# Kernel optimization log

Hardware: AMD Instinct MI355X
Metric: run time of the kernel (lower is better)

The kernel has to match this reference:

```python
import jax, jax.numpy as jnp
import numpy as np
from math import sqrt

B, L, D, H, DK, IN = 128, 256, 128, 4, 64, 40
N = B * L
E = 524288
NLAYERS = 4
DISW = 1.5
EPS = 1e-5


def _ln(x, g, b):
    mu = x.mean(-1, keepdims=True)
    v = ((x - mu) ** 2).mean(-1, keepdims=True)
    return (x - mu) / jnp.sqrt(v + EPS) * g + b


def setup_inputs() -> dict:
    key = jax.random.key(0)
    ks = jax.random.split(key, 32)
    x = jax.random.normal(ks[0], (N, IN), jnp.float32)
    # equal-sized graphs: graph g owns nodes [g*L, (g+1)*L)
    e_per = E // B
    off = (jnp.arange(E) // e_per) * L
    src = off + jax.random.randint(ks[1], (E,), 0, L)
    dst = off + jax.random.randint(ks[2], (E,), 0, L)
    edge_index = jnp.stack([src, dst]).astype(jnp.int32)
    edge_attr = jax.random.uniform(ks[3], (E,), jnp.float32)
    # adjacency-type matrix with entries in {0, 1, 1.2} as in the source's adj semantics
    a = jax.random.randint(ks[4], (B, L, L), 0, 3)
    adj = jnp.where(a == 2, 1.2, a.astype(jnp.float32))
    dis = jax.random.randint(ks[5], (B, L, L), 0, 7).astype(jnp.float32)
    mask = jnp.ones((B, L), dtype=bool)  # all graphs have length L -> no padding
    s = 0.05
    p = {}
    p['gnn0_rel_w'] = jax.random.normal(ks[6], (IN, D)) * s
    p['gnn0_rel_b'] = jnp.zeros((D,), jnp.float32)
    p['gnn0_root_w'] = jax.random.normal(ks[7], (IN, D)) * s
    p['gnn_rel_w'] = jax.random.normal(ks[8], (NLAYERS - 1, D, D)) * s
    p['gnn_rel_b'] = jnp.zeros((NLAYERS - 1, D), jnp.float32)
    p['gnn_root_w'] = jax.random.normal(ks[9], (NLAYERS - 1, D, D)) * s
    p['nm_g'] = jnp.ones((NLAYERS, D), jnp.float32)
    p['nm_b'] = jnp.zeros((NLAYERS, D), jnp.float32)
    p['wq'] = jax.random.normal(ks[10], (NLAYERS, D, H * DK)) * s
    p['wk'] = jax.random.normal(ks[11], (NLAYERS, D, H * DK)) * s
    p['wv'] = jax.random.normal(ks[12], (NLAYERS, D, H * DK)) * s
    p['fc'] = jax.random.normal(ks[13], (NLAYERS, H * DK, D)) * s
    p['mha_ln_g'] = jnp.ones((NLAYERS, D), jnp.float32)
    p['mha_ln_b'] = jnp.zeros((NLAYERS, D), jnp.float32)
    p['enc_ln_g'] = jnp.ones((NLAYERS, D), jnp.float32)
    p['enc_ln_b'] = jnp.zeros((NLAYERS, D), jnp.float32)
    p['proj_w'] = jax.random.normal(ks[14], (D, D)) * s
    p['proj_b'] = jnp.zeros((D,), jnp.float32)
    return dict(x=x, edge_index=edge_index, edge_attr=edge_attr, adj=adj, dis=dis, mask=mask, **p)


def _graph_conv(x, src, dst, ew, rel_w, rel_b, root_w):
    # torch_geometric GraphConv: lin_rel(sum_j e_ji * x_j) + lin_root(x_i)
    msg = ew[:, None] * x[src]
    agg = jax.ops.segment_sum(msg, dst, num_segments=N)
    return agg @ rel_w + rel_b + x @ root_w


def _encoder(xb, pad, matrix, wq, wk, wv, fc, mg, mb, eg, eb):
    q = (xb @ wq).reshape(B, L, H, DK).transpose(0, 2, 1, 3)  # [B,H,L,dk]
    k = (xb @ wk).reshape(B, L, H, DK).transpose(0, 2, 1, 3)
    v = (xb @ wv).reshape(B, L, H, DK).transpose(0, 2, 1, 3)
    scores = jnp.einsum('bhqd,bhkd->bhqk', q, k) / sqrt(DK) * matrix[:, None]
    scores = jnp.where(pad[:, None, None, :], -1e9, scores)
    attn = jax.nn.softmax(scores, axis=-1)
    ctx = jnp.einsum('bhqk,bhkd->bhqd', attn, v).transpose(0, 2, 1, 3).reshape(B, L, H * DK)
    out = _ln(ctx @ fc, mg, mb)  # MHA output LayerNorm (dropout is eval -> identity)
    return _ln(out + xb, eg, eb)  # EncoderLayer residual + LayerNorm


def reference(x, edge_index, edge_attr, adj, dis, mask,
              gnn0_rel_w, gnn0_rel_b, gnn0_root_w,
              gnn_rel_w, gnn_rel_b, gnn_root_w,
              nm_g, nm_b, wq, wk, wv, fc,
              mha_ln_g, mha_ln_b, enc_ln_g, enc_ln_b,
              proj_w, proj_b):
    src, dst = edge_index[0], edge_index[1]
    # matrix construction (done once; same matrix_pad reused every layer)
    adj_ = jnp.where(adj == 1.2, 1.1, adj)
    dis_ = jnp.where(dis == 0.0, 0.0, 1.0 / jnp.power(DISW, dis - 1.0))
    matrix = jnp.where(adj == 0.0, dis_, adj_)  # [B,L,L]
    pad = ~mask  # key padding mask (True = masked); all-False here
    h = x
    for i in range(NLAYERS):
        rw = gnn0_rel_w if i == 0 else gnn_rel_w[i - 1]
        rb = gnn0_rel_b if i == 0 else gnn_rel_b[i - 1]
        ow = gnn0_root_w if i == 0 else gnn_root_w[i - 1]
        h = _graph_conv(h, src, dst, edge_attr, rw, rb, ow)
        h = jax.nn.relu(_ln(h, nm_g[i], nm_b[i]))
        xb = h.reshape(B, L, D)  # to_dense_batch with equal lengths
        xb = _encoder(xb, pad, matrix, wq[i], wk[i], wv[i], fc[i],
                      mha_ln_g[i], mha_ln_b[i], enc_ln_g[i], enc_ln_b[i])
        h = xb.reshape(N, D)  # masked_select back to node list
    return h @ proj_w + proj_b
```

## Files before the change

### kernel.cpp

```cpp
#include <hip/hip_runtime.h>
#include <stdint.h>

typedef unsigned short u16;
typedef unsigned int u32;
typedef __attribute__((ext_vector_type(4))) float f32x4;
typedef __attribute__((ext_vector_type(8))) short bf16x8;

#define NB 128
#define LL 256
#define DD 128
#define EDGES 524288
#define EPG 4096
#define NN (NB*LL)

__device__ __forceinline__ float bf2f(u16 u) {
    union { u32 i; float f; } v; v.i = ((u32)u) << 16; return v.f;
}
__device__ __forceinline__ u16 f2bf(float f) {
    union { float f; u32 i; } v; v.f = f;
    u32 i = v.i;
    u32 r = (i + 0x7fffu + ((i >> 16) & 1u)) >> 16;
    return (u16)r;
}
__device__ __forceinline__ float matfn(float a, float dv) {
    if (a != 0.f) return (a == 1.2f) ? 1.1f : a;
    return (dv == 0.f) ? 0.f : exp2f((1.f - dv) * 0.5849625007211562f);
}
__device__ __forceinline__ float red16(float v) {
#pragma unroll
    for (int off = 1; off < 16; off <<= 1) v += __shfl_xor(v, off, 64);
    return v;
}
__device__ __forceinline__ u32 cvtpk(float lo, float hi) {
    u32 r;
    asm("v_cvt_pk_bf16_f32 %0, %1, %2" : "=v"(r) : "v"(lo), "v"(hi));
    return r;
}
__device__ __forceinline__ u32 bperm(int srcLane, u32 v) {
    return (u32)__builtin_amdgcn_ds_bpermute(srcLane << 2, (int)v);
}


__global__ __launch_bounds__(256) void scatter_w_k(const int* __restrict__ srcI,
                                                   const int* __restrict__ dstI,
                                                   const float* __restrict__ ew,
                                                   float* __restrict__ Wf) {
    int e = blockIdx.x * 256 + threadIdx.x;
    if (e >= EDGES) return;
    int b = e >> 12;
    atomicAdd(&Wf[(size_t)b * 65536 + (size_t)(dstI[e] & 255) * 256 + (srcI[e] & 255)], ew[e]);
}

__global__ __launch_bounds__(256) void cast_w_k(const float* __restrict__ Wf, u16* __restrict__ Wb) {
    int i = blockIdx.x * 256 + threadIdx.x;
    float4 v = ((const float4*)Wf)[i];
    ushort4 o;
    o.x = f2bf(v.x); o.y = f2bf(v.y); o.z = f2bf(v.z); o.w = f2bf(v.w);
    ((ushort4*)Wb)[i] = o;
}

__global__ __launch_bounds__(256) void build_matrix_k(const float* __restrict__ adj,
                                                      const float* __restrict__ dis,
                                                      float* __restrict__ mat) {
    int i = blockIdx.x * 256 + threadIdx.x;
    mat[i] = 0.125f * matfn(adj[i], dis[i]);
}

__global__ __launch_bounds__(256) void prep_weights_k(
        const float* __restrict__ g0_rel_w, const float* __restrict__ g0_root_w,
        const float* __restrict__ g_rel_w,  const float* __restrict__ g_root_w,
        const float* __restrict__ wq, const float* __restrict__ wk,
        const float* __restrict__ wv, const float* __restrict__ fc,
        const float* __restrict__ proj_w,
        u16* __restrict__ wconvT0, u16* __restrict__ wconvT,
        u16* __restrict__ wqkvT, u16* __restrict__ fcT, u16* __restrict__ projT) {
    int i = blockIdx.x * 256 + threadIdx.x;
    if (i < 16384) {
        int m = i >> 7, k = i & 127;
        float v = 0.f;
        if (k < 40) v = g0_rel_w[k * 128 + m];
        else if (k >= 64 && k < 104) v = g0_root_w[(k - 64) * 128 + m];
        wconvT0[i] = f2bf(v);
        return;
    }
    i -= 16384;
    if (i < 98304) {
        int l = i >> 15, jj = i & 32767;
        int m = jj >> 8, k = jj & 255;
        float v = (k < 128) ? g_rel_w[l * 16384 + k * 128 + m]
                            : g_root_w[l * 16384 + (k - 128) * 128 + m];
        wconvT[i] = f2bf(v);
        return;
    }
    i -= 98304;
    if (i < 393216) {
        int l = i / 98304, jj = i % 98304;
        int m = jj >> 7, k = jj & 127;
        const float* s = (m < 256) ? wq : (m < 512) ? wk : wv;
        int mm = m & 255;
        wqkvT[i] = f2bf(s[l * 32768 + k * 256 + mm]);
        return;
    }
    i -= 393216;
    if (i < 131072) {
        int l = i >> 15, jj = i & 32767;
        int m = jj >> 8, k = jj & 255;
        fcT[i] = f2bf(fc[l * 32768 + k * 128 + m]);
        return;
    }
    i -= 131072;
    {
        int m = i >> 7, k = i & 127;
        projT[i] = f2bf(proj_w[k * 128 + m]);
    }
}

__global__ __launch_bounds__(256) void transpose_x_k(const float* __restrict__ x,
                                                     u16* __restrict__ hT) {
    int gw = blockIdx.x * 4 + (threadIdx.x >> 6);
    int lane = threadIdx.x & 63;
    int b = gw >> 6, rem = gw & 63, db = rem >> 5, jb = rem & 31;
    int d = (db << 6) + lane;
    u16 vals[8];
#pragma unroll
    for (int jj = 0; jj < 8; ++jj) {
        int node = (b << 8) + (jb << 3) + jj;
        vals[jj] = (d < 40) ? f2bf(x[(size_t)node * 40 + d]) : (u16)0;
    }
    *(uint4*)(hT + (size_t)b * 32768 + (size_t)d * 256 + (jb << 3)) = *(uint4*)vals;
}


template<bool IS0>
__global__ __launch_bounds__(256) void gemm_agg(const u16* __restrict__ Wb,
                                                const u16* __restrict__ BT0,
                                                const float* __restrict__ x,
                                                u16* __restrict__ Aagg) {
    __shared__ __align__(16) u16 lds[8192];
    char* ldsc = (char*)lds;
    int t = threadIdx.x, lane = t & 63, wid = t >> 6;
    int b = blockIdx.x >> 1, rt = blockIdx.x & 1;
    int row0 = rt << 7, nbase = b << 8;
    const u16* A = Wb + (size_t)b * 65536 + (size_t)row0 * 256;
    const u16* BT = BT0 + (size_t)b * 32768;

    f32x4 zero = {0.f, 0.f, 0.f, 0.f};
    f32x4 acc[4][4];
#pragma unroll
    for (int mt = 0; mt < 4; ++mt)
#pragma unroll
        for (int nt = 0; nt < 4; ++nt) acc[mt][nt] = zero;

    int wr = wid >> 1, wc = wid & 1;
    int rA = wr * 64 + (lane & 15);
    int rB = wc * 64 + (lane & 15);
    int kch = (lane >> 4) << 4;

    for (int kt = 0; kt < 8; ++kt) {
        int kc = kt << 5;
#pragma unroll
        for (int i = 0; i < 2; ++i) {
            int off = wid * 2048 + i * 1024 + lane * 16;
            int r = off >> 6, cb = off & 63;
            __builtin_amdgcn_global_load_lds((const u32*)((const char*)A + ((size_t)r * 256 + kc) * 2 + cb),
                                             (u32*)(ldsc + wid * 2048 + i * 1024), 16, 0, 0);
            __builtin_amdgcn_global_load_lds((const u32*)((const char*)BT + ((size_t)r * 256 + kc) * 2 + cb),
                                             (u32*)(ldsc + 8192 + wid * 2048 + i * 1024), 16, 0, 0);
        }
        __syncthreads();
        bf16x8 af[4], bfr[4];
#pragma unroll
        for (int mt = 0; mt < 4; ++mt)
            af[mt] = *(const bf16x8*)(ldsc + (rA + mt * 16) * 64 + kch);
#pragma unroll
        for (int nt = 0; nt < 4; ++nt)
            bfr[nt] = *(const bf16x8*)(ldsc + 8192 + (rB + nt * 16) * 64 + kch);
#pragma unroll
        for (int mt = 0; mt < 4; ++mt)
#pragma unroll
            for (int nt = 0; nt < 4; ++nt)
                acc[mt][nt] = __builtin_amdgcn_mfma_f32_16x16x32_bf16(af[mt], bfr[nt], acc[mt][nt], 0, 0, 0);
        __syncthreads();
    }

    int colb = wc * 64 + (lane & 15);
    int rowb = wr * 64 + ((lane >> 4) << 2);
#pragma unroll
    for (int mt = 0; mt < 4; ++mt)
#pragma unroll
        for (int nt = 0; nt < 4; ++nt)
#pragma unroll
            for (int r = 0; r < 4; ++r)
                Aagg[(size_t)(nbase + row0 + rowb + mt * 16 + r) * 128 + colb + nt * 16]
                    = f2bf(acc[mt][nt][r]);
    if (IS0) {
        for (int idx = t; idx < 128 * 40; idx += 256) {
            int i = idx / 40, c = idx - i * 40;
            int node = nbase + row0 + i;
            Aagg[(size_t)node * 128 + 64 + c] = f2bf(x[(size_t)node * 40 + c]);
        }
    }
}


__global__ __launch_bounds__(256) void gemm_qkv(const u16* __restrict__ A,
                                                const u16* __restrict__ BT,
                                                u16* __restrict__ qP,
                                                u16* __restrict__ kP,
                                                u16* __restrict__ vT) {
    __shared__ __align__(16) u16 lds[8192];
    char* ldsc = (char*)lds;
    int t = threadIdx.x, lane = t & 63, wid = t >> 6;
    int row0 = blockIdx.x * 128, col0 = blockIdx.y * 128;

    f32x4 zero = {0.f, 0.f, 0.f, 0.f};
    f32x4 acc[4][4];
#pragma unroll
    for (int mt = 0; mt < 4; ++mt)
#pragma unroll
        for (int nt = 0; nt < 4; ++nt) acc[mt][nt] = zero;

    int wr = wid >> 1, wc = wid & 1;
    int rA = wr * 64 + (lane & 15);
    int rB = wc * 64 + (lane & 15);
    int kch = (lane >> 4) << 4;

    for (int kt = 0; kt < 4; ++kt) {
        int kc = kt << 5;
#pragma unroll
        for (int i = 0; i < 2; ++i) {
            int off = wid * 2048 + i * 1024 + lane * 16;
            int r = off >> 6, cb = off & 63;
            __builtin_amdgcn_global_load_lds((const u32*)((const char*)A + ((size_t)(row0 + r) * 128 + kc) * 2 + cb),
                                             (u32*)(ldsc + wid * 2048 + i * 1024), 16, 0, 0);
            __builtin_amdgcn_global_load_lds((const u32*)((const char*)BT + ((size_t)(col0 + r) * 128 + kc) * 2 + cb),
                                             (u32*)(ldsc + 8192 + wid * 2048 + i * 1024), 16, 0, 0);
        }
        __syncthreads();
        bf16x8 af[4], bfr[4];
#pragma unroll
        for (int mt = 0; mt < 4; ++mt)
            af[mt] = *(const bf16x8*)(ldsc + (rA + mt * 16) * 64 + kch);
#pragma unroll
        for (int nt = 0; nt < 4; ++nt)
            bfr[nt] = *(const bf16x8*)(ldsc + 8192 + (rB + nt * 16) * 64 + kch);
#pragma unroll
        for (int mt = 0; mt < 4; ++mt)
#pragma unroll
            for (int nt = 0; nt < 4; ++nt)
                acc[mt][nt] = __builtin_amdgcn_mfma_f32_16x16x32_bf16(af[mt], bfr[nt], acc[mt][nt], 0, 0, 0);
        __syncthreads();
    }

    int colb = col0 + wc * 64 + (lane & 15);
    int rowb = row0 + wr * 64 + ((lane >> 4) << 2);
    int bb = row0 >> 8;
    if (col0 < 512) {
        u16* dst = (col0 < 256) ? qP : kP;
#pragma unroll
        for (int mt = 0; mt < 4; ++mt) {
#pragma unroll
            for (int nt = 0; nt < 4; ++nt) {
                int c = (colb + nt * 16) & 255;
                int hh = c >> 6, d = c & 63;
#pragma unroll
                for (int r = 0; r < 4; ++r) {
                    int node = (rowb + mt * 16 + r) & 255;
                    dst[(size_t)(bb * 4 + hh) * 16384 + node * 64 + d] = f2bf(acc[mt][nt][r]);
                }
            }
        }
    } else {
#pragma unroll
        for (int mt = 0; mt < 4; ++mt) {
            int node0 = (rowb + mt * 16) & 255;
#pragma unroll
            for (int nt = 0; nt < 4; ++nt) {
                int c = colb + nt * 16 - 512;
                int hh = c >> 6, d = c & 63;
                u16 tmp[4];
#pragma unroll
                for (int r = 0; r < 4; ++r) tmp[r] = f2bf(acc[mt][nt][r]);
                *(ushort4*)(vT + (size_t)(bb * 4 + hh) * 16384 + d * 256 + node0) = *(ushort4*)tmp;
            }
        }
    }
}


__global__ __launch_bounds__(256) void gemm_proj(const u16* __restrict__ A,
                                                 const u16* __restrict__ BT,
                                                 float* __restrict__ Out,
                                                 const float* __restrict__ bias) {
    __shared__ __align__(16) u16 lds[8192];
    char* ldsc = (char*)lds;
    int t = threadIdx.x, lane = t & 63, wid = t >> 6;
    int row0 = blockIdx.x * 128;

    f32x4 zero = {0.f, 0.f, 0.f, 0.f};
    f32x4 acc[4][4];
#pragma unroll
    for (int mt = 0; mt < 4; ++mt)
#pragma unroll
        for (int nt = 0; nt < 4; ++nt) acc[mt][nt] = zero;

    int wr = wid >> 1, wc = wid & 1;
    int rA = wr * 64 + (lane & 15);
    int rB = wc * 64 + (lane & 15);
    int kch = (lane >> 4) << 4;

    for (int kt = 0; kt < 4; ++kt) {
        int kc = kt << 5;
#pragma unroll
        for (int i = 0; i < 2; ++i) {
            int off = wid * 2048 + i * 1024 + lane * 16;
            int r = off >> 6, cb = off & 63;
            __builtin_amdgcn_global_load_lds((const u32*)((const char*)A + ((size_t)(row0 + r) * 128 + kc) * 2 + cb),
                                             (u32*)(ldsc + wid * 2048 + i * 1024), 16, 0, 0);
            __builtin_amdgcn_global_load_lds((const u32*)((const char*)BT + ((size_t)r * 128 + kc) * 2 + cb),
                                             (u32*)(ldsc + 8192 + wid * 2048 + i * 1024), 16, 0, 0);
        }
        __syncthreads();
        bf16x8 af[4], bfr[4];
#pragma unroll
        for (int mt = 0; mt < 4; ++mt)
            af[mt] = *(const bf16x8*)(ldsc + (rA + mt * 16) * 64 + kch);
#pragma unroll
        for (int nt = 0; nt < 4; ++nt)
            bfr[nt] = *(const bf16x8*)(ldsc + 8192 + (rB + nt * 16) * 64 + kch);
#pragma unroll
        for (int mt = 0; mt < 4; ++mt)
#pragma unroll
            for (int nt = 0; nt < 4; ++nt)
                acc[mt][nt] = __builtin_amdgcn_mfma_f32_16x16x32_bf16(af[mt], bfr[nt], acc[mt][nt], 0, 0, 0);
        __syncthreads();
    }

    int colb = wc * 64 + (lane & 15);
    int rowb = row0 + wr * 64 + ((lane >> 4) << 2);
#pragma unroll
    for (int mt = 0; mt < 4; ++mt)
#pragma unroll
        for (int nt = 0; nt < 4; ++nt)
#pragma unroll
            for (int r = 0; r < 4; ++r)
                Out[(size_t)(rowb + mt * 16 + r) * 128 + colb + nt * 16] =
                    acc[mt][nt][r] + bias[colb + nt * 16];
}


__global__ __launch_bounds__(256) void gemm_conv_ln0(const u16* __restrict__ A,
                                                     const u16* __restrict__ BT,
                                                     const float* __restrict__ rb,
                                                     const float* __restrict__ g,
                                                     const float* __restrict__ be,
                                                     u16* __restrict__ hout) {
    __shared__ __align__(16) u16 lds[8192];
    char* ldsc = (char*)lds;
    int t = threadIdx.x, lane = t & 63, wid = t >> 6;
    int row0 = blockIdx.x * 128;

    f32x4 zero = {0.f, 0.f, 0.f, 0.f};
    f32x4 acc[4][4];
#pragma unroll
    for (int mt = 0; mt < 4; ++mt)
#pragma unroll
        for (int nt = 0; nt < 4; ++nt) acc[mt][nt] = zero;

    int wr = wid >> 1, wc = wid & 1;
    int rA = wr * 64 + (lane & 15);
    int rB = wc * 64 + (lane & 15);
    int kch = (lane >> 4) << 4;

    for (int kt = 0; kt < 4; ++kt) {
        int kc = kt << 5;
#pragma unroll
        for (int i = 0; i < 2; ++i) {
            int off = wid * 2048 + i * 1024 + lane * 16;
            int r = off >> 6, cb = off & 63;
            __builtin_amdgcn_global_load_lds((const u32*)((const char*)A + ((size_t)(row0 + r) * 128 + kc) * 2 + cb),
                                             (u32*)(ldsc + wid * 2048 + i * 1024), 16, 0, 0);
            __builtin_amdgcn_global_load_lds((const u32*)((const char*)BT + ((size_t)r * 128 + kc) * 2 + cb),
                                             (u32*)(ldsc + 8192 + wid * 2048 + i * 1024), 16, 0, 0);
        }
        __syncthreads();
        bf16x8 af[4], bfr[4];
#pragma unroll
        for (int mt = 0; mt < 4; ++mt)
            af[mt] = *(const bf16x8*)(ldsc + (rA + mt * 16) * 64 + kch);
#pragma unroll
        for (int nt = 0; nt < 4; ++nt)
            bfr[nt] = *(const bf16x8*)(ldsc + 8192 + (rB + nt * 16) * 64 + kch);
#pragma unroll
        for (int mt = 0; mt < 4; ++mt)
#pragma unroll
            for (int nt = 0; nt < 4; ++nt)
                acc[mt][nt] = __builtin_amdgcn_mfma_f32_16x16x32_bf16(af[mt], bfr[nt], acc[mt][nt], 0, 0, 0);
        __syncthreads();
    }

    float* redS = (float*)ldsc;
    float* redQ = (float*)(ldsc + 2048);
    int colbase = wc * 64 + (lane & 15);
    int qrow = (lane >> 4) << 2;
    float rbv[4], gv[4], bev[4];
#pragma unroll
    for (int nt = 0; nt < 4; ++nt) {
        int c = colbase + nt * 16;
        rbv[nt] = rb[c]; gv[nt] = g[c]; bev[nt] = be[c];
    }
#pragma unroll
    for (int mt = 0; mt < 4; ++mt)
#pragma unroll
        for (int r = 0; r < 4; ++r) {
            float s = 0.f, q = 0.f;
#pragma unroll
            for (int nt = 0; nt < 4; ++nt) {
                float v = acc[mt][nt][r] + rbv[nt];
                s += v; q += v * v;
            }
            s = red16(s); q = red16(q);
            if ((lane & 15) == 0) {
                int lr = wr * 64 + qrow + mt * 16 + r;
                redS[lr * 2 + wc] = s; redQ[lr * 2 + wc] = q;
            }
        }
    __syncthreads();
#pragma unroll
    for (int mt = 0; mt < 4; ++mt)
#pragma unroll
        for (int r = 0; r < 4; ++r) {
            int lr = wr * 64 + qrow + mt * 16 + r;
            float mu = (redS[lr * 2] + redS[lr * 2 + 1]) * (1.f / 128.f);
            float var = (redQ[lr * 2] + redQ[lr * 2 + 1]) * (1.f / 128.f) - mu * mu;
            float rs = rsqrtf(var + 1e-5f);
            size_t rbase = (size_t)(row0 + lr) * 128;
#pragma unroll
            for (int nt = 0; nt < 4; ++nt) {
                float v = acc[mt][nt][r] + rbv[nt];
                float o = (v - mu) * rs * gv[nt] + bev[nt];
                o = o < 0.f ? 0.f : o;
                hout[rbase + colbase + nt * 16] = f2bf(o);
            }
        }
}


__global__ __launch_bounds__(256) void gemm_conv_ln_split(const u16* __restrict__ Aagg,
                                                          u16* h,
                                                          const u16* __restrict__ BT,
                                                          const float* __restrict__ rb,
                                                          const float* __restrict__ g,
                                                          const float* __restrict__ be) {
    __shared__ __align__(16) u16 lds[8192];
    char* ldsc = (char*)lds;
    int t = threadIdx.x, lane = t & 63, wid = t >> 6;
    int row0 = blockIdx.x * 128;

    f32x4 zero = {0.f, 0.f, 0.f, 0.f};
    f32x4 acc[4][4];
#pragma unroll
    for (int mt = 0; mt < 4; ++mt)
#pragma unroll
        for (int nt = 0; nt < 4; ++nt) acc[mt][nt] = zero;

    int wr = wid >> 1, wc = wid & 1;
    int rA = wr * 64 + (lane & 15);
    int rB = wc * 64 + (lane & 15);
    int kch = (lane >> 4) << 4;

    for (int kt = 0; kt < 8; ++kt) {
        const u16* Abase = (kt < 4) ? Aagg : (const u16*)h;
        int kcl = (kt & 3) << 5;
        int kc = kt << 5;
#pragma unroll
        for (int i = 0; i < 2; ++i) {
            int off = wid * 2048 + i * 1024 + lane * 16;
            int r = off >> 6, cb = off & 63;
            __builtin_amdgcn_global_load_lds((const u32*)((const char*)Abase + ((size_t)(row0 + r) * 128 + kcl) * 2 + cb),
                                             (u32*)(ldsc + wid * 2048 + i * 1024), 16, 0, 0);
            __builtin_amdgcn_global_load_lds((const u32*)((const char*)BT + ((size_t)r * 256 + kc) * 2 + cb),
                                             (u32*)(ldsc + 8192 + wid * 2048 + i * 1024), 16, 0, 0);
        }
        __syncthreads();
        bf16x8 af[4], bfr[4];
#pragma unroll
        for (int mt = 0; mt < 4; ++mt)
            af[mt] = *(const bf16x8*)(ldsc + (rA + mt * 16) * 64 + kch);
#pragma unroll
        for (int nt = 0; nt < 4; ++nt)
            bfr[nt] = *(const bf16x8*)(ldsc + 8192 + (rB + nt * 16) * 64 + kch);
#pragma unroll
        for (int mt = 0; mt < 4; ++mt)
#pragma unroll
            for (int nt = 0; nt < 4; ++nt)
                acc[mt][nt] = __builtin_amdgcn_mfma_f32_16x16x32_bf16(af[mt], bfr[nt], acc[mt][nt], 0, 0, 0);
        __syncthreads();
    }

    float* redS = (float*)ldsc;
    float* redQ = (float*)(ldsc + 2048);
    int colbase = wc * 64 + (lane & 15);
    int qrow = (lane >> 4) << 2;
    float rbv[4], gv[4], bev[4];
#pragma unroll
    for (int nt = 0; nt < 4; ++nt) {
        int c = colbase + nt * 16;
        rbv[nt] = rb[c]; gv[nt] = g[c]; bev[nt] = be[c];
    }
#pragma unroll
    for (int mt = 0; mt < 4; ++mt)
#pragma unroll
        for (int r = 0; r < 4; ++r) {
            float s = 0.f, q = 0.f;
#pragma unroll
            for (int nt = 0; nt < 4; ++nt) {
                float v = acc[mt][nt][r] + rbv[nt];
                s += v; q += v * v;
            }
            s = red16(s); q = red16(q);
            if ((lane & 15) == 0) {
                int lr = wr * 64 + qrow + mt * 16 + r;
                redS[lr * 2 + wc] = s; redQ[lr * 2 + wc] = q;
            }
        }
    __syncthreads();
#pragma unroll
    for (int mt = 0; mt < 4; ++mt)
#pragma unroll
        for (int r = 0; r < 4; ++r) {
            int lr = wr * 64 + qrow + mt * 16 + r;
            float mu = (redS[lr * 2] + redS[lr * 2 + 1]) * (1.f / 128.f);
            float var = (redQ[lr * 2] + redQ[lr * 2 + 1]) * (1.f / 128.f) - mu * mu;
            float rs = rsqrtf(var + 1e-5f);
            size_t rbase = (size_t)(row0 + lr) * 128;
#pragma unroll
            for (int nt = 0; nt < 4; ++nt) {
                float v = acc[mt][nt][r] + rbv[nt];
                float o = (v - mu) * rs * gv[nt] + bev[nt];
                o = o < 0.f ? 0.f : o;
                h[rbase + colbase + nt * 16] = f2bf(o);
            }
        }
}


__global__ __launch_bounds__(256) void gemm_fc_ln2(const u16* __restrict__ A,
                                                   const u16* __restrict__ BT,
                                                   const float* __restrict__ mg,
                                                   const float* __restrict__ mb,
                                                   const float* __restrict__ eg,
                                                   const float* __restrict__ eb,
                                                   u16* __restrict__ h,
                                                   u16* __restrict__ hT) {
    __shared__ __align__(16) u16 lds[8192];
    char* ldsc = (char*)lds;
    int t = threadIdx.x, lane = t & 63, wid = t >> 6;
    int row0 = blockIdx.x * 128;

    f32x4 zero = {0.f, 0.f, 0.f, 0.f};
    f32x4 acc[4][4];
#pragma unroll
    for (int mt = 0; mt < 4; ++mt)
#pragma unroll
        for (int nt = 0; nt < 4; ++nt) acc[mt][nt] = zero;

    int wr = wid >> 1, wc = wid & 1;
    int rA = wr * 64 + (lane & 15);
    int rB = wc * 64 + (lane & 15);
    int kch = (lane >> 4) << 4;

    for (int kt = 0; kt < 8; ++kt) {
        int kc = kt << 5;
#pragma unroll
        for (int i = 0; i < 2; ++i) {
            int off = wid * 2048 + i * 1024 + lane * 16;
            int r = off >> 6, cb = off & 63;
            __builtin_amdgcn_global_load_lds((const u32*)((const char*)A + ((size_t)(row0 + r) * 256 + kc) * 2 + cb),
                                             (u32*)(ldsc + wid * 2048 + i * 1024), 16, 0, 0);
            __builtin_amdgcn_global_load_lds((const u32*)((const char*)BT + ((size_t)r * 256 + kc) * 2 + cb),
                                             (u32*)(ldsc + 8192 + wid * 2048 + i * 1024), 16, 0, 0);
        }
        __syncthreads();
        bf16x8 af[4], bfr[4];
#pragma unroll
        for (int mt = 0; mt < 4; ++mt)
            af[mt] = *(const bf16x8*)(ldsc + (rA + mt * 16) * 64 + kch);
#pragma unroll
        for (int nt = 0; nt < 4; ++nt)
            bfr[nt] = *(const bf16x8*)(ldsc + 8192 + (rB + nt * 16) * 64 + kch);
#pragma unroll
        for (int mt = 0; mt < 4; ++mt)
#pragma unroll
            for (int nt = 0; nt < 4; ++nt)
                acc[mt][nt] = __builtin_amdgcn_mfma_f32_16x16x32_bf16(af[mt], bfr[nt], acc[mt][nt], 0, 0, 0);
        __syncthreads();
    }

    float* redS  = (float*)ldsc;
    float* redQ  = (float*)(ldsc + 2048);
    float* redS2 = (float*)(ldsc + 4096);
    float* redQ2 = (float*)(ldsc + 6144);
    int colbase = wc * 64 + (lane & 15);
    int qrow = (lane >> 4) << 2;
    float mgv[4], mbv[4], egv[4], ebv[4];
#pragma unroll
    for (int nt = 0; nt < 4; ++nt) {
        int c = colbase + nt * 16;
        mgv[nt] = mg[c]; mbv[nt] = mb[c]; egv[nt] = eg[c]; ebv[nt] = eb[c];
    }
#pragma unroll
    for (int mt = 0; mt < 4; ++mt)
#pragma unroll
        for (int r = 0; r < 4; ++r) {
            float s = 0.f, q = 0.f;
#pragma unroll
            for (int nt = 0; nt < 4; ++nt) {
                float v = acc[mt][nt][r];
                s += v; q += v * v;
            }
            s = red16(s); q = red16(q);
            if ((lane & 15) == 0) {
                int lr = wr * 64 + qrow + mt * 16 + r;
                redS[lr * 2 + wc] = s; redQ[lr * 2 + wc] = q;
            }
        }
    __syncthreads();
#pragma unroll
    for (int mt = 0; mt < 4; ++mt)
#pragma unroll
        for (int r = 0; r < 4; ++r) {
            int lr = wr * 64 + qrow + mt * 16 + r;
            float mu = (redS[lr * 2] + redS[lr * 2 + 1]) * (1.f / 128.f);
            float var = (redQ[lr * 2] + redQ[lr * 2 + 1]) * (1.f / 128.f) - mu * mu;
            float rs = rsqrtf(var + 1e-5f);
            size_t rbase = (size_t)(row0 + lr) * 128;
            float s2 = 0.f, q2 = 0.f;
#pragma unroll
            for (int nt = 0; nt < 4; ++nt) {
                float o = (acc[mt][nt][r] - mu) * rs * mgv[nt] + mbv[nt];
                float z = o + bf2f(h[rbase + colbase + nt * 16]);
                acc[mt][nt][r] = z;
                s2 += z; q2 += z * z;
            }
            s2 = red16(s2); q2 = red16(q2);
            if ((lane & 15) == 0) {
                redS2[lr * 2 + wc] = s2; redQ2[lr * 2 + wc] = q2;
            }
        }
    __syncthreads();
    int bb = row0 >> 8;
#pragma unroll
    for (int mt = 0; mt < 4; ++mt) {
        u16 tvals[4][4];
#pragma unroll
        for (int r = 0; r < 4; ++r) {
            int lr = wr * 64 + qrow + mt * 16 + r;
            float mu = (redS2[lr * 2] + redS2[lr * 2 + 1]) * (1.f / 128.f);
            float var = (redQ2[lr * 2] + redQ2[lr * 2 + 1]) * (1.f / 128.f) - mu * mu;
            float rs = rsqrtf(var + 1e-5f);
            size_t rbase = (size_t)(row0 + lr) * 128;
#pragma unroll
            for (int nt = 0; nt < 4; ++nt) {
                float z = acc[mt][nt][r];
                u16 o = f2bf((z - mu) * rs * egv[nt] + ebv[nt]);
                h[rbase + colbase + nt * 16] = o;
                tvals[nt][r] = o;
            }
        }
        int node0 = ((row0 & 255) + wr * 64 + qrow + mt * 16);
#pragma unroll
        for (int nt = 0; nt < 4; ++nt) {
            int d = colbase + nt * 16;
            *(ushort4*)(hT + (size_t)bb * 32768 + (size_t)d * 256 + node0) = *(ushort4*)tvals[nt];
        }
    }
}


__global__ __launch_bounds__(512) void attn_k(const u16* __restrict__ qP,
                                              const u16* __restrict__ kP,
                                              const u16* __restrict__ vT,
                                              const float* __restrict__ mat,
                                              u16* __restrict__ ctx) {
    __shared__ __align__(16) u16 Kl[256 * 72];
    __shared__ __align__(16) u16 Vl[64 * 264];
    int t = threadIdx.x, lane = t & 63, w = t >> 6;
    int b = blockIdx.x, hh = blockIdx.y;
    int bh = b * 4 + hh;
    int lg = lane >> 4, q16 = lane & 15;

    {
        const u16* kb = kP + (size_t)bh * 16384;
#pragma unroll
        for (int i = 0; i < 4; ++i) {
            int idx = i * 512 + t;
            int node = idx >> 3, oct = idx & 7;
            *(uint4*)(Kl + node * 72 + oct * 8) = *(const uint4*)(kb + node * 64 + oct * 8);
        }
        const u16* vb = vT + (size_t)bh * 16384;
#pragma unroll
        for (int i = 0; i < 4; ++i) {
            int idx = i * 512 + t;
            int d = idx >> 5, p = idx & 31;
            *(uint4*)(Vl + d * 264 + p * 8) = *(const uint4*)(vb + d * 256 + p * 8);
        }
    }
    __syncthreads();

    f32x4 zero = {0.f, 0.f, 0.f, 0.f};
    bool loA = (lg < 2);
    int s01 = q16 + ((lg & 1) << 5);
    int s23 = s01 + 16;

    for (int qi = 0; qi < 2; ++qi) {
        int qrow_l = w * 32 + qi * 16;

        const u16* qsrc = qP + (size_t)bh * 16384 + (qrow_l + q16) * 64 + (lg << 3);
        bf16x8 aq0 = *(const bf16x8*)(qsrc);
        bf16x8 aq1 = *(const bf16x8*)(qsrc + 32);

        f32x4 sc[16];
#pragma unroll
        for (int nt = 0; nt < 16; ++nt) {
            const u16* ks = Kl + (nt * 16 + q16) * 72 + (lg << 3);
            bf16x8 k0 = *(const bf16x8*)(ks);
            bf16x8 k1 = *(const bf16x8*)(ks + 32);
            f32x4 a = __builtin_amdgcn_mfma_f32_16x16x32_bf16(k0, aq0, zero, 0, 0, 0);
            a = __builtin_amdgcn_mfma_f32_16x16x32_bf16(k1, aq1, a, 0, 0, 0);
            sc[nt] = a;
        }

        const float* mrow = mat + ((size_t)b * LL + qrow_l + q16) * LL + (lg << 2);
#pragma unroll
        for (int nt = 0; nt < 16; ++nt) {
            f32x4 mv = *(const f32x4*)(mrow + nt * 16);
#pragma unroll
            for (int r = 0; r < 4; ++r)
                sc[nt][r] *= mv[r];
        }

        float mx = -1e30f;
#pragma unroll
        for (int nt = 0; nt < 16; ++nt)
#pragma unroll
            for (int r = 0; r < 4; ++r) mx = fmaxf(mx, sc[nt][r]);
        mx = fmaxf(mx, __shfl_xor(mx, 16, 64));
        mx = fmaxf(mx, __shfl_xor(mx, 32, 64));
        float sm = 0.f;
#pragma unroll
        for (int nt = 0; nt < 16; ++nt)
#pragma unroll
            for (int r = 0; r < 4; ++r) {
                float e = __expf(sc[nt][r] - mx);
                sc[nt][r] = e;
                sm += e;
            }
        sm += __shfl_xor(sm, 16, 64);
        sm += __shfl_xor(sm, 32, 64);
        float inv = 1.f / sm;
#pragma unroll
        for (int nt = 0; nt < 16; ++nt)
#pragma unroll
            for (int r = 0; r < 4; ++r) sc[nt][r] *= inv;

        f32x4 oa[4];
#pragma unroll
        for (int dt = 0; dt < 4; ++dt) oa[dt] = zero;
#pragma unroll
        for (int kt = 0; kt < 8; ++kt) {
            u32 A0 = cvtpk(sc[2 * kt][0], sc[2 * kt][1]);
            u32 A1 = cvtpk(sc[2 * kt][2], sc[2 * kt][3]);
            u32 B0 = cvtpk(sc[2 * kt + 1][0], sc[2 * kt + 1][1]);
            u32 B1 = cvtpk(sc[2 * kt + 1][2], sc[2 * kt + 1][3]);
            u32 a0s = bperm(s01, A0), b0s = bperm(s01, B0);
            u32 a1s = bperm(s01, A1), b1s = bperm(s01, B1);
            u32 a0t = bperm(s23, A0), b0t = bperm(s23, B0);
            u32 a1t = bperm(s23, A1), b1t = bperm(s23, B1);
            union { u32 u[4]; bf16x8 v; } pa;
            pa.u[0] = loA ? a0s : b0s;
            pa.u[1] = loA ? a1s : b1s;
            pa.u[2] = loA ? a0t : b0t;
            pa.u[3] = loA ? a1t : b1t;
#pragma unroll
            for (int dt = 0; dt < 4; ++dt) {
                bf16x8 bv = *(const bf16x8*)(Vl + (dt * 16 + q16) * 264 + kt * 32 + (lg << 3));
                oa[dt] = __builtin_amdgcn_mfma_f32_16x16x32_bf16(pa.v, bv, oa[dt], 0, 0, 0);
            }
        }
#pragma unroll
        for (int dt = 0; dt < 4; ++dt)
#pragma unroll
            for (int r = 0; r < 4; ++r)
                ctx[(size_t)(b * LL + qrow_l + (lg << 2) + r) * 256 + hh * 64 + dt * 16 + q16] = f2bf(oa[dt][r]);
    }
}


extern "C" void kernel_launch(void* const* d_in, const int* in_sizes, int n_in,
                              void* d_out, int out_size, void* d_ws, size_t ws_size,
                              hipStream_t stream) {
    (void)out_size; (void)ws_size; (void)n_in;
    const float* x        = (const float*)d_in[0];
    const int*   ei       = (const int*)d_in[1];
    const float* ea       = (const float*)d_in[2];
    const float* adj      = (const float*)d_in[3];
    const float* dis      = (const float*)d_in[4];
    int pb = (in_sizes[5] == 5120) ? 5 : 6;
    const float* g0_rel_w = (const float*)d_in[pb + 0];
    const float* g0_rel_b = (const float*)d_in[pb + 1];
    const float* g0_root_w= (const float*)d_in[pb + 2];
    const float* g_rel_w  = (const float*)d_in[pb + 3];
    const float* g_rel_b  = (const float*)d_in[pb + 4];
    const float* g_root_w = (const float*)d_in[pb + 5];
    const float* nm_g     = (const float*)d_in[pb + 6];
    const float* nm_b     = (const float*)d_in[pb + 7];
    const float* wq       = (const float*)d_in[pb + 8];
    const float* wk       = (const float*)d_in[pb + 9];
    const float* wv       = (const float*)d_in[pb + 10];
    const float* fc       = (const float*)d_in[pb + 11];
    const float* mha_g    = (const float*)d_in[pb + 12];
    const float* mha_b    = (const float*)d_in[pb + 13];
    const float* enc_g    = (const float*)d_in[pb + 14];
    const float* enc_b    = (const float*)d_in[pb + 15];
    const float* proj_w   = (const float*)d_in[pb + 16];
    const float* proj_b   = (const float*)d_in[pb + 17];
    const int* srcI = ei;
    const int* dstI = ei + EDGES;

    char* w = (char*)d_ws;
    float* Wf     = (float*)w; w += (size_t)33554432;
    u16*   Acat   = (u16*)w;   w += (size_t)16777216;
    u16*   h      = (u16*)w;   w += (size_t)8388608;
    u16*   qP     = (u16*)w;   w += (size_t)16777216;
    u16*   kP     = (u16*)w;   w += (size_t)16777216;
    u16*   Wb     = (u16*)w;   w += (size_t)16777216;
    u16*   bigT   = (u16*)w;   w += (size_t)16777216;
    u16* wconvT0  = (u16*)w;   w += (size_t)32768;
    u16* wconvT   = (u16*)w;   w += (size_t)196608;
    u16* wqkvT    = (u16*)w;   w += (size_t)786432;
    u16* fcT      = (u16*)w;   w += (size_t)262144;
    u16* projT    = (u16*)w;   w += (size_t)32768;
    float* mat = Wf;
    u16*   ctx = Acat;
    u16*   hT  = bigT;
    u16*   vT  = bigT;

    hipMemsetAsync(Wf, 0, 33554432, stream);
    scatter_w_k<<<2048, 256, 0, stream>>>(srcI, dstI, ea, Wf);
    cast_w_k<<<8192, 256, 0, stream>>>(Wf, Wb);
    build_matrix_k<<<32768, 256, 0, stream>>>(adj, dis, mat);
    prep_weights_k<<<2560, 256, 0, stream>>>(g0_rel_w, g0_root_w, g_rel_w, g_root_w,
                                             wq, wk, wv, fc, proj_w,
                                             wconvT0, wconvT, wqkvT, fcT, projT);
    transpose_x_k<<<2048, 256, 0, stream>>>(x, hT);

    for (int L = 0; L < 4; ++L) {
        if (L == 0) {
            gemm_agg<true><<<256, 256, 0, stream>>>(Wb, hT, x, Acat);
            gemm_conv_ln0<<<256, 256, 0, stream>>>(Acat, wconvT0, g0_rel_b, nm_g, nm_b, h);
        } else {
            gemm_agg<false><<<256, 256, 0, stream>>>(Wb, hT, x, Acat);
            gemm_conv_ln_split<<<256, 256, 0, stream>>>(Acat, h, wconvT + (L - 1) * 32768,
                                                        g_rel_b + (L - 1) * 128,
                                                        nm_g + L * 128, nm_b + L * 128);
        }
        gemm_qkv<<<dim3(256, 6), 256, 0, stream>>>(h, wqkvT + L * 98304, qP, kP, vT);
        attn_k<<<dim3(NB, 4), 512, 0, stream>>>(qP, kP, vT, mat, ctx);
        gemm_fc_ln2<<<256, 256, 0, stream>>>(ctx, fcT + L * 32768,
                                             mha_g + L * 128, mha_b + L * 128,
                                             enc_g + L * 128, enc_b + L * 128, h, hT);
    }
    gemm_proj<<<256, 256, 0, stream>>>(h, projT, (float*)d_out, proj_b);
}
```

Measured before the change: 521.6 us.

## Fuse aggregation GEMM with conv GEMM+LayerNorm and store attention matrix in bf16

The aggregation GEMM output now stays in LDS and feeds directly into the conv GEMM, bias, LayerNorm and ReLU inside one kernel. This removes the intermediate Acat round trip through global memory and one launch per layer. Separately, the attention bias matrix is stored as bf16 instead of fp32, halving its read traffic in attn_k at some cost in precision. The larger LDS footprint may reduce occupancy.

```diff
diff --git a/kernel.cpp b/kernel.cpp
--- a/kernel.cpp
+++ b/kernel.cpp
@@ -61,9 +61,9 @@
 
 __global__ __launch_bounds__(256) void build_matrix_k(const float* __restrict__ adj,
                                                       const float* __restrict__ dis,
-                                                      float* __restrict__ mat) {
+                                                      u16* __restrict__ matB) {
     int i = blockIdx.x * 256 + threadIdx.x;
-    mat[i] = 0.125f * matfn(adj[i], dis[i]);
+    matB[i] = f2bf(0.125f * matfn(adj[i], dis[i]));
 }
 
 __global__ __launch_bounds__(256) void prep_weights_k(
@@ -132,12 +132,17 @@
 
 
 template<bool IS0>
-__global__ __launch_bounds__(256) void gemm_agg(const u16* __restrict__ Wb,
-                                                const u16* __restrict__ BT0,
-                                                const float* __restrict__ x,
-                                                u16* __restrict__ Aagg) {
-    __shared__ __align__(16) u16 lds[8192];
+__global__ __launch_bounds__(256) void gemm_agg_conv(const u16* __restrict__ Wb,
+                                                     const u16* __restrict__ BT0,
+                                                     const float* __restrict__ x,
+                                                     u16* h,
+                                                     const u16* __restrict__ BTc,
+                                                     const float* __restrict__ rb,
+                                                     const float* __restrict__ g,
+                                                     const float* __restrict__ be) {
+    __shared__ __align__(16) u16 lds[8192 + 128 * 136];
     char* ldsc = (char*)lds;
+    u16* aggT = lds + 8192;
     int t = threadIdx.x, lane = t & 63, wid = t >> 6;
     int b = blockIdx.x >> 1, rt = blockIdx.x & 1;
     int row0 = rt << 7, nbase = b << 8;
@@ -183,23 +188,113 @@
         __syncthreads();
     }
 
-    int colb = wc * 64 + (lane & 15);
-    int rowb = wr * 64 + ((lane >> 4) << 2);
-#pragma unroll
-    for (int mt = 0; mt < 4; ++mt)
+    {
+        int colb = wc * 64 + (lane & 15);
+        int rowb = wr * 64 + ((lane >> 4) << 2);
+#pragma unroll
+        for (int mt = 0; mt < 4; ++mt)
+#pragma unroll
+            for (int nt = 0; nt < 4; ++nt)
+#pragma unroll
+                for (int r = 0; r < 4; ++r)
+                    aggT[(rowb + mt * 16 + r) * 136 + colb + nt * 16] = f2bf(acc[mt][nt][r]);
+        if (IS0) {
+            for (int idx = t; idx < 128 * 40; idx += 256) {
+                int i = idx / 40, c = idx - i * 40;
+                aggT[i * 136 + 64 + c] = f2bf(x[(size_t)(nbase + row0 + i) * 40 + c]);
+            }
+        }
+    }
+    __syncthreads();
+
+#pragma unroll
+    for (int mt = 0; mt < 4; ++mt)
+#pragma unroll
+        for (int nt = 0; nt < 4; ++nt) acc[mt][nt] = zero;
+
+    const int NKT = IS0 ? 4 : 8;
+    const int KK = IS0 ? 128 : 256;
+    for (int kt = 0; kt < NKT; ++kt) {
+        int kc = kt << 5;
+        bool fromLds = IS0 || (kt < 4);
+#pragma unroll
+        for (int i = 0; i < 2; ++i) {
+            int off = wid * 2048 + i * 1024 + lane * 16;
+            int r = off >> 6, cb = off & 63;
+            if (!fromLds) {
+                int kcl = (kt - 4) << 5;
+                __builtin_amdgcn_global_load_lds((const u32*)((const char*)h + ((size_t)(nbase + row0 + r) * 128 + kcl) * 2 + cb),
+                                                 (u32*)(ldsc + wid * 2048 + i * 1024), 16, 0, 0);
+            }
+            __builtin_amdgcn_global_load_lds((const u32*)((const char*)BTc + ((size_t)r * KK + kc) * 2 + cb),
+                                             (u32*)(ldsc + 8192 + wid * 2048 + i * 1024), 16, 0, 0);
+        }
+        __syncthreads();
+        bf16x8 af[4], bfr[4];
+        if (fromLds) {
+#pragma unroll
+            for (int mt = 0; mt < 4; ++mt)
+                af[mt] = *(const bf16x8*)((const char*)aggT + (rA + mt * 16) * 272 + kt * 64 + kch);
+        } else {
+#pragma unroll
+            for (int mt = 0; mt < 4; ++mt)
+                af[mt] = *(const bf16x8*)(ldsc + (rA + mt * 16) * 64 + kch);
+        }
 #pragma unroll
         for (int nt = 0; nt < 4; ++nt)
-#pragma unroll
-            for (int r = 0; r < 4; ++r)
-                Aagg[(size_t)(nbase + row0 + rowb + mt * 16 + r) * 128 + colb + nt * 16]
-                    = f2bf(acc[mt][nt][r]);
-    if (IS0) {
-        for (int idx = t; idx < 128 * 40; idx += 256) {
-            int i = idx / 40, c = idx - i * 40;
-            int node = nbase + row0 + i;
-            Aagg[(size_t)node * 128 + 64 + c] = f2bf(x[(size_t)node * 40 + c]);
-        }
-    }
+            bfr[nt] = *(const bf16x8*)(ldsc + 8192 + (rB + nt * 16) * 64 + kch);
+#pragma unroll
+        for (int mt = 0; mt < 4; ++mt)
+#pragma unroll
+            for (int nt = 0; nt < 4; ++nt)
+                acc[mt][nt] = __builtin_amdgcn_mfma_f32_16x16x32_bf16(af[mt], bfr[nt], acc[mt][nt], 0, 0, 0);
+        __syncthreads();
+    }
+
+    float* redS = (float*)ldsc;
+    float* redQ = (float*)(ldsc + 2048);
+    int colbase = wc * 64 + (lane & 15);
+    int qrow = (lane >> 4) << 2;
+    float rbv[4], gv[4], bev[4];
+#pragma unroll
+    for (int nt = 0; nt < 4; ++nt) {
+        int c = colbase + nt * 16;
+        rbv[nt] = rb[c]; gv[nt] = g[c]; bev[nt] = be[c];
+    }
+#pragma unroll
+    for (int mt = 0; mt < 4; ++mt)
+#pragma unroll
+        for (int r = 0; r < 4; ++r) {
+            float s = 0.f, q = 0.f;
+#pragma unroll
+            for (int nt = 0; nt < 4; ++nt) {
+                float v = acc[mt][nt][r] + rbv[nt];
+                s += v; q += v * v;
+            }
+            s = red16(s); q = red16(q);
+            if ((lane & 15) == 0) {
+                int lr = wr * 64 + qrow + mt * 16 + r;
+                redS[lr * 2 + wc] = s; redQ[lr * 2 + wc] = q;
+            }
+        }
+    __syncthreads();
+#pragma unroll
+    for (int mt = 0; mt < 4; ++mt)
+#pragma unroll
+        for (int r = 0; r < 4; ++r) {
+            int lr = wr * 64 + qrow + mt * 16 + r;
+            float mu = (redS[lr * 2] + redS[lr * 2 + 1]) * (1.f / 128.f);
+            float var = (redQ[lr * 2] + redQ[lr * 2 + 1]) * (1.f / 128.f) - mu * mu;
+            float rs = rsqrtf(var + 1e-5f);
+            size_t rbase = (size_t)(nbase + row0 + lr) * 128;
+#pragma unroll
+            for (int nt = 0; nt < 4; ++nt) {
+                float v = acc[mt][nt][r] + rbv[nt];
+                float o = (v - mu) * rs * gv[nt] + bev[nt];
+                o = o < 0.f ? 0.f : o;
+                h[rbase + colbase + nt * 16] = f2bf(o);
+            }
+        }
 }
 
 
@@ -346,202 +441,6 @@
             for (int r = 0; r < 4; ++r)
                 Out[(size_t)(rowb + mt * 16 + r) * 128 + colb + nt * 16] =
                     acc[mt][nt][r] + bias[colb + nt * 16];
-}
-
-
-__global__ __launch_bounds__(256) void gemm_conv_ln0(const u16* __restrict__ A,
-                                                     const u16* __restrict__ BT,
-                                                     const float* __restrict__ rb,
-                                                     const float* __restrict__ g,
-                                                     const float* __restrict__ be,
-                                                     u16* __restrict__ hout) {
-    __shared__ __align__(16) u16 lds[8192];
-    char* ldsc = (char*)lds;
-    int t = threadIdx.x, lane = t & 63, wid = t >> 6;
-    int row0 = blockIdx.x * 128;
-
-    f32x4 zero = {0.f, 0.f, 0.f, 0.f};
-    f32x4 acc[4][4];
-#pragma unroll
-    for (int mt = 0; mt < 4; ++mt)
-#pragma unroll
-        for (int nt = 0; nt < 4; ++nt) acc[mt][nt] = zero;
-
-    int wr = wid >> 1, wc = wid & 1;
-    int rA = wr * 64 + (lane & 15);
-    int rB = wc * 64 + (lane & 15);
-    int kch = (lane >> 4) << 4;
-
-    for (int kt = 0; kt < 4; ++kt) {
-        int kc = kt << 5;
-#pragma unroll
-        for (int i = 0; i < 2; ++i) {
-            int off = wid * 2048 + i * 1024 + lane * 16;
-            int r = off >> 6, cb = off & 63;
-            __builtin_amdgcn_global_load_lds((const u32*)((const char*)A + ((size_t)(row0 + r) * 128 + kc) * 2 + cb),
-                                             (u32*)(ldsc + wid * 2048 + i * 1024), 16, 0, 0);
-            __builtin_amdgcn_global_load_lds((const u32*)((const char*)BT + ((size_t)r * 128 + kc) * 2 + cb),
-                                             (u32*)(ldsc + 8192 + wid * 2048 + i * 1024), 16, 0, 0);
-        }
-        __syncthreads();
-        bf16x8 af[4], bfr[4];
-#pragma unroll
-        for (int mt = 0; mt < 4; ++mt)
-            af[mt] = *(const bf16x8*)(ldsc + (rA + mt * 16) * 64 + kch);
-#pragma unroll
-        for (int nt = 0; nt < 4; ++nt)
-            bfr[nt] = *(const bf16x8*)(ldsc + 8192 + (rB + nt * 16) * 64 + kch);
-#pragma unroll
-        for (int mt = 0; mt < 4; ++mt)
-#pragma unroll
-            for (int nt = 0; nt < 4; ++nt)
-                acc[mt][nt] = __builtin_amdgcn_mfma_f32_16x16x32_bf16(af[mt], bfr[nt], acc[mt][nt], 0, 0, 0);
-        __syncthreads();
-    }
-
-    float* redS = (float*)ldsc;
-    float* redQ = (float*)(ldsc + 2048);
-    int colbase = wc * 64 + (lane & 15);
-    int qrow = (lane >> 4) << 2;
-    float rbv[4], gv[4], bev[4];
-#pragma unroll
-    for (int nt = 0; nt < 4; ++nt) {
-        int c = colbase + nt * 16;
-        rbv[nt] = rb[c]; gv[nt] = g[c]; bev[nt] = be[c];
-    }
-#pragma unroll
-    for (int mt = 0; mt < 4; ++mt)
-#pragma unroll
-        for (int r = 0; r < 4; ++r) {
-            float s = 0.f, q = 0.f;
-#pragma unroll
-            for (int nt = 0; nt < 4; ++nt) {
-                float v = acc[mt][nt][r] + rbv[nt];
-                s += v; q += v * v;
-            }
-            s = red16(s); q = red16(q);
-            if ((lane & 15) == 0) {
-                int lr = wr * 64 + qrow + mt * 16 + r;
-                redS[lr * 2 + wc] = s; redQ[lr * 2 + wc] = q;
-            }
-        }
-    __syncthreads();
-#pragma unroll
-    for (int mt = 0; mt < 4; ++mt)
-#pragma unroll
-        for (int r = 0; r < 4; ++r) {
-            int lr = wr * 64 + qrow + mt * 16 + r;
-            float mu = (redS[lr * 2] + redS[lr * 2 + 1]) * (1.f / 128.f);
-            float var = (redQ[lr * 2] + redQ[lr * 2 + 1]) * (1.f / 128.f) - mu * mu;
-            float rs = rsqrtf(var + 1e-5f);
-            size_t rbase = (size_t)(row0 + lr) * 128;
-#pragma unroll
-            for (int nt = 0; nt < 4; ++nt) {
-                float v = acc[mt][nt][r] + rbv[nt];
-                float o = (v - mu) * rs * gv[nt] + bev[nt];
-                o = o < 0.f ? 0.f : o;
-                hout[rbase + colbase + nt * 16] = f2bf(o);
-            }
-        }
-}
-
-
-__global__ __launch_bounds__(256) void gemm_conv_ln_split(const u16* __restrict__ Aagg,
-                                                          u16* h,
-                                                          const u16* __restrict__ BT,
-                                                          const float* __restrict__ rb,
-                                                          const float* __restrict__ g,
-                                                          const float* __restrict__ be) {
-    __shared__ __align__(16) u16 lds[8192];
-    char* ldsc = (char*)lds;
-    int t = threadIdx.x, lane = t & 63, wid = t >> 6;
-    int row0 = blockIdx.x * 128;
-
-    f32x4 zero = {0.f, 0.f, 0.f, 0.f};
-    f32x4 acc[4][4];
-#pragma unroll
-    for (int mt = 0; mt < 4; ++mt)
-#pragma unroll
-        for (int nt = 0; nt < 4; ++nt) acc[mt][nt] = zero;
-
-    int wr = wid >> 1, wc = wid & 1;
-    int rA = wr * 64 + (lane & 15);
-    int rB = wc * 64 + (lane & 15);
-    int kch = (lane >> 4) << 4;
-
-    for (int kt = 0; kt < 8; ++kt) {
-        const u16* Abase = (kt < 4) ? Aagg : (const u16*)h;
-        int kcl = (kt & 3) << 5;
-        int kc = kt << 5;
-#pragma unroll
-        for (int i = 0; i < 2; ++i) {
-            int off = wid * 2048 + i * 1024 + lane * 16;
-            int r = off >> 6, cb = off & 63;
-            __builtin_amdgcn_global_load_lds((const u32*)((const char*)Abase + ((size_t)(row0 + r) * 128 + kcl) * 2 + cb),
-                                             (u32*)(ldsc + wid * 2048 + i * 1024), 16, 0, 0);
-            __builtin_amdgcn_global_load_lds((const u32*)((const char*)BT + ((size_t)r * 256 + kc) * 2 + cb),
-                                             (u32*)(ldsc + 8192 + wid * 2048 + i * 1024), 16, 0, 0);
-        }
-        __syncthreads();
-        bf16x8 af[4], bfr[4];
-#pragma unroll
-        for (int mt = 0; mt < 4; ++mt)
-            af[mt] = *(const bf16x8*)(ldsc + (rA + mt * 16) * 64 + kch);
-#pragma unroll
-        for (int nt = 0; nt < 4; ++nt)
-            bfr[nt] = *(const bf16x8*)(ldsc + 8192 + (rB + nt * 16) * 64 + kch);
-#pragma unroll
-        for (int mt = 0; mt < 4; ++mt)
-#pragma unroll
-            for (int nt = 0; nt < 4; ++nt)
-                acc[mt][nt] = __builtin_amdgcn_mfma_f32_16x16x32_bf16(af[mt], bfr[nt], acc[mt][nt], 0, 0, 0);
-        __syncthreads();
-    }
-
-    float* redS = (float*)ldsc;
-    float* redQ = (float*)(ldsc + 2048);
-    int colbase = wc * 64 + (lane & 15);
-    int qrow = (lane >> 4) << 2;
-    float rbv[4], gv[4], bev[4];
-#pragma unroll
-    for (int nt = 0; nt < 4; ++nt) {
-        int c = colbase + nt * 16;
-        rbv[nt] = rb[c]; gv[nt] = g[c]; bev[nt] = be[c];
-    }
-#pragma unroll
-    for (int mt = 0; mt < 4; ++mt)
-#pragma unroll
-        for (int r = 0; r < 4; ++r) {
-            float s = 0.f, q = 0.f;
-#pragma unroll
-            for (int nt = 0; nt < 4; ++nt) {
-                float v = acc[mt][nt][r] + rbv[nt];
-                s += v; q += v * v;
-            }
-            s = red16(s); q = red16(q);
-            if ((lane & 15) == 0) {
-                int lr = wr * 64 + qrow + mt * 16 + r;
-                redS[lr * 2 + wc] = s; redQ[lr * 2 + wc] = q;
-            }
-        }
-    __syncthreads();
-#pragma unroll
-    for (int mt = 0; mt < 4; ++mt)
-#pragma unroll
-        for (int r = 0; r < 4; ++r) {
-            int lr = wr * 64 + qrow + mt * 16 + r;
-            float mu = (redS[lr * 2] + redS[lr * 2 + 1]) * (1.f / 128.f);
-            float var = (redQ[lr * 2] + redQ[lr * 2 + 1]) * (1.f / 128.f) - mu * mu;
-            float rs = rsqrtf(var + 1e-5f);
-            size_t rbase = (size_t)(row0 + lr) * 128;
-#pragma unroll
-            for (int nt = 0; nt < 4; ++nt) {
-                float v = acc[mt][nt][r] + rbv[nt];
-                float o = (v - mu) * rs * gv[nt] + bev[nt];
-                o = o < 0.f ? 0.f : o;
-                h[rbase + colbase + nt * 16] = f2bf(o);
-            }
-        }
 }
 
 
@@ -681,7 +580,7 @@
 __global__ __launch_bounds__(512) void attn_k(const u16* __restrict__ qP,
                                               const u16* __restrict__ kP,
                                               const u16* __restrict__ vT,
-                                              const float* __restrict__ mat,
+                                              const u16* __restrict__ matB,
                                               u16* __restrict__ ctx) {
     __shared__ __align__(16) u16 Kl[256 * 72];
     __shared__ __align__(16) u16 Vl[64 * 264];
@@ -731,13 +630,14 @@
             sc[nt] = a;
         }
 
-        const float* mrow = mat + ((size_t)b * LL + qrow_l + q16) * LL + (lg << 2);
+        const u16* mrow = matB + ((size_t)b * LL + qrow_l + q16) * LL + (lg << 2);
 #pragma unroll
         for (int nt = 0; nt < 16; ++nt) {
-            f32x4 mv = *(const f32x4*)(mrow + nt * 16);
-#pragma unroll
-            for (int r = 0; r < 4; ++r)
-                sc[nt][r] *= mv[r];
+            ushort4 mv = *(const ushort4*)(mrow + nt * 16);
+            sc[nt][0] *= bf2f(mv.x);
+            sc[nt][1] *= bf2f(mv.y);
+            sc[nt][2] *= bf2f(mv.z);
+            sc[nt][3] *= bf2f(mv.w);
         }
 
         float mx = -1e30f;
@@ -830,7 +730,7 @@
 
     char* w = (char*)d_ws;
     float* Wf     = (float*)w; w += (size_t)33554432;
-    u16*   Acat   = (u16*)w;   w += (size_t)16777216;
+    u16*   ctx    = (u16*)w;   w += (size_t)16777216;
     u16*   h      = (u16*)w;   w += (size_t)8388608;
     u16*   qP     = (u16*)w;   w += (size_t)16777216;
     u16*   kP     = (u16*)w;   w += (size_t)16777216;
@@ -841,32 +741,29 @@
     u16* wqkvT    = (u16*)w;   w += (size_t)786432;
     u16* fcT      = (u16*)w;   w += (size_t)262144;
     u16* projT    = (u16*)w;   w += (size_t)32768;
-    float* mat = Wf;
-    u16*   ctx = Acat;
+    u16*   matB = (u16*)Wf;
     u16*   hT  = bigT;
     u16*   vT  = bigT;
 
     hipMemsetAsync(Wf, 0, 33554432, stream);
     scatter_w_k<<<2048, 256, 0, stream>>>(srcI, dstI, ea, Wf);
     cast_w_k<<<8192, 256, 0, stream>>>(Wf, Wb);
-    build_matrix_k<<<32768, 256, 0, stream>>>(adj, dis, mat);
+    build_matrix_k<<<32768, 256, 0, stream>>>(adj, dis, matB);
     prep_weights_k<<<2560, 256, 0, stream>>>(g0_rel_w, g0_root_w, g_rel_w, g_root_w,
                                              wq, wk, wv, fc, proj_w,
                                              wconvT0, wconvT, wqkvT, fcT, projT);
     transpose_x_k<<<2048, 256, 0, stream>>>(x, hT);
 
     for (int L = 0; L < 4; ++L) {
-        if (L == 0) {
-            gemm_agg<true><<<256, 256, 0, stream>>>(Wb, hT, x, Acat);
-            gemm_conv_ln0<<<256, 256, 0, stream>>>(Acat, wconvT0, g0_rel_b, nm_g, nm_b, h);
-        } else {
-            gemm_agg<false><<<256, 256, 0, stream>>>(Wb, hT, x, Acat);
-            gemm_conv_ln_split<<<256, 256, 0, stream>>>(Acat, h, wconvT + (L - 1) * 32768,
-                                                        g_rel_b + (L - 1) * 128,
-                                                        nm_g + L * 128, nm_b + L * 128);
-        }
+        if (L == 0)
+            gemm_agg_conv<true><<<256, 256, 0, stream>>>(Wb, hT, x, h, wconvT0,
+                                                         g0_rel_b, nm_g, nm_b);
+        else
+            gemm_agg_conv<false><<<256, 256, 0, stream>>>(Wb, hT, x, h, wconvT + (L - 1) * 32768,
+                                                          g_rel_b + (L - 1) * 128,
+                                                          nm_g + L * 128, nm_b + L * 128);
         gemm_qkv<<<dim3(256, 6), 256, 0, stream>>>(h, wqkvT + L * 98304, qP, kP, vT);
-        attn_k<<<dim3(NB, 4), 512, 0, stream>>>(qP, kP, vT, mat, ctx);
+        attn_k<<<dim3(NB, 4), 512, 0, stream>>>(qP, kP, vT, matB, ctx);
         gemm_fc_ln2<<<256, 256, 0, stream>>>(ctx, fcT + L * 32768,
                                              mha_g + L * 128, mha_b + L * 128,
                                              enc_g + L * 128, enc_b + L * 128, h, hT);
```

New measurement: 505.7 us. -3.0%, faster.
